# Performance work log

Hardware: AMD Instinct MI355X
Metric: run time of the kernel (lower is better)

The kernel has to match this reference:

```python
import jax, jax.numpy as jnp
import numpy as np

LAMBDA_INIT = 0.8


def setup_inputs() -> dict:
    key = jax.random.key(0)
    ks = jax.random.split(key, 12)
    B, T, E = 2, 2048, 1024
    H = 8            # num_heads // 2 diff-heads
    HS = 64          # head_size
    DO = 128         # 2 * head_output_dimension (per-head output dim)
    q = jax.random.normal(ks[0], (B, T, E), jnp.float32)
    k = jax.random.normal(ks[1], (B, T, E), jnp.float32)
    v = jax.random.normal(ks[2], (B, T, E), jnp.float32)
    s = E ** -0.5  # linear-layer style init scale
    Wq = jax.random.normal(ks[3], (H, E, 2 * HS), jnp.float32) * s
    Wk = jax.random.normal(ks[4], (H, E, 2 * HS), jnp.float32) * s
    Wv = jax.random.normal(ks[5], (H, E, DO), jnp.float32) * s
    # lambda reparam vectors (scaled 0.1 to keep exp(dot) numerically tame)
    lq1 = jax.random.normal(ks[6], (H, HS), jnp.float32) * 0.1
    lk1 = jax.random.normal(ks[7], (H, HS), jnp.float32) * 0.1
    lq2 = jax.random.normal(ks[8], (H, HS), jnp.float32) * 0.1
    lk2 = jax.random.normal(ks[9], (H, HS), jnp.float32) * 0.1
    Wp = jax.random.normal(ks[10], (H * DO, E), jnp.float32) * (H * DO) ** -0.5
    bp = jnp.zeros((E,), jnp.float32)
    # buffer: tril(ones, diagonal=1); positions where it is 0 get -inf
    mask = jnp.tril(jnp.ones((T, T), jnp.bool_), 1)
    return {"q": q, "k": k, "v": v, "Wq": Wq, "Wk": Wk, "Wv": Wv,
            "lq1": lq1, "lk1": lk1, "lq2": lq2, "lk2": lk2,
            "Wp": Wp, "bp": bp, "mask": mask}


def reference(q, k, v, Wq, Wk, Wv, lq1, lk1, lq2, lk2, Wp, bp, mask):
    B, T, E = q.shape
    H = Wq.shape[0]
    HS = Wq.shape[-1] // 2
    scale = HS ** -0.5
    Q = jnp.einsum('bte,hed->bhtd', q, Wq)   # [B,H,T,2HS]
    K = jnp.einsum('bte,hed->bhtd', k, Wk)
    V = jnp.einsum('bte,hed->bhtd', v, Wv)   # [B,H,T,DO]
    Q1, Q2 = jnp.split(Q, 2, axis=-1)
    K1, K2 = jnp.split(K, 2, axis=-1)
    neg_inf = jnp.float32(-jnp.inf)
    s1 = jnp.einsum('bhtd,bhsd->bhts', Q1, K1) * scale
    s2 = jnp.einsum('bhtd,bhsd->bhts', Q2, K2) * scale
    s1 = jnp.where(mask[:T, :T], s1, neg_inf)
    s2 = jnp.where(mask[:T, :T], s2, neg_inf)
    a1 = jax.nn.softmax(s1, axis=-1)
    a2 = jax.nn.softmax(s2, axis=-1)
    lbd = (jnp.exp(jnp.sum(lq1 * lk1, -1)) - jnp.exp(jnp.sum(lq2 * lk2, -1))
           + LAMBDA_INIT)                     # [H]
    attn = a1 - lbd[None, :, None, None] * a2
    ctx = jnp.einsum('bhts,bhsd->bhtd', attn, V) * (1.0 - LAMBDA_INIT)
    out = ctx.transpose(0, 2, 1, 3).reshape(B, T, -1)  # concat heads
    return out @ Wp + bp
```

## Files before the change

kernel.cpp:

```cpp
#include <hip/hip_runtime.h>
#include <hip/hip_bf16.h>


constexpr int Tn = 2048;
constexpr int En = 1024;
constexpr int Hn = 8;
constexpr float LAMBDA_INIT = 0.8f;
constexpr float QSCALE = 0.18033688011112042f;

typedef __attribute__((ext_vector_type(8))) short short8;
typedef __attribute__((ext_vector_type(4))) short s16x4;
typedef __attribute__((ext_vector_type(4))) float f32x4;

__device__ __forceinline__ short f2bf(float x) {
  union { __hip_bfloat16 h; short s; } u;
  u.h = __float2bfloat16(x);
  return u.s;
}
__device__ __forceinline__ void gload16(const short* g, short* l) {
  __builtin_amdgcn_global_load_lds(
      (const __attribute__((address_space(1))) void*)g,
      (__attribute__((address_space(3))) void*)l, 16, 0, 0);
}

__global__ __launch_bounds__(256)
void qkv_mfma(const float* __restrict__ q, const float* __restrict__ k,
              const float* __restrict__ v,
              const float* __restrict__ Wq, const float* __restrict__ Wk,
              const float* __restrict__ Wv,
              short* __restrict__ Qo, short* __restrict__ Ko,
              short* __restrict__ Vto) {
  __shared__ short As[128 * 32];
  __shared__ short Bs[128 * 32];
  const int which = blockIdx.z;
  const float* X = (which == 0) ? q : (which == 1) ? k : v;
  const float* W = (which == 0) ? Wq : (which == 1) ? Wk : Wv;
  const int head = blockIdx.y;
  const int m0 = blockIdx.x * 128;
  const float* Wh = W + (size_t)head * En * 128;
  const float oscale = (which == 0) ? QSCALE : 1.0f;

  const int tid = threadIdx.x;
  const int lane = tid & 63;
  const int w = tid >> 6, wr = w >> 1, wc = w & 1;
  const int fr = lane & 15, fk = (lane >> 4) * 8;
  const int arow = tid >> 1, ah = (tid & 1) * 16;
  const int bn = tid & 127, bkg = (tid >> 7) * 16;

  f32x4 acc[4][4] = {};

  for (int k0 = 0; k0 < En; k0 += 32) {
    float4 xa[4];
#pragma unroll
    for (int qq = 0; qq < 4; ++qq)
      xa[qq] = *(const float4*)&X[(size_t)(m0 + arow) * En + k0 + ah + qq * 4];
    float xb[16];
#pragma unroll
    for (int j = 0; j < 16; ++j)
      xb[j] = Wh[(size_t)(k0 + bkg + j) * 128 + bn];

    __syncthreads();
    short8 pa0, pa1;
#pragma unroll
    for (int e = 0; e < 4; ++e) {
      pa0[e]     = f2bf(((const float*)&xa[0])[e]);
      pa0[e + 4] = f2bf(((const float*)&xa[1])[e]);
      pa1[e]     = f2bf(((const float*)&xa[2])[e]);
      pa1[e + 4] = f2bf(((const float*)&xa[3])[e]);
    }
    *(short8*)&As[arow * 32 + ah] = pa0;
    *(short8*)&As[arow * 32 + ah + 8] = pa1;
    short8 pb0, pb1;
#pragma unroll
    for (int e = 0; e < 8; ++e) {
      pb0[e] = f2bf(xb[e]);
      pb1[e] = f2bf(xb[e + 8]);
    }
    *(short8*)&Bs[bn * 32 + bkg] = pb0;
    *(short8*)&Bs[bn * 32 + bkg + 8] = pb1;
    __syncthreads();

    short8 a[4], b[4];
#pragma unroll
    for (int i = 0; i < 4; ++i)
      a[i] = *(const short8*)&As[(wr * 64 + i * 16 + fr) * 32 + fk];
#pragma unroll
    for (int j = 0; j < 4; ++j)
      b[j] = *(const short8*)&Bs[(wc * 64 + j * 16 + fr) * 32 + fk];
#pragma unroll
    for (int i = 0; i < 4; ++i)
#pragma unroll
      for (int j = 0; j < 4; ++j)
        acc[i][j] = __builtin_amdgcn_mfma_f32_16x16x32_bf16(a[i], b[j],
                                                            acc[i][j], 0, 0, 0);
  }

  const int crow = (lane >> 4) * 4, ccol = lane & 15;
  if (which == 2) {
#pragma unroll
    for (int i = 0; i < 4; ++i) {
      const int m = m0 + wr * 64 + i * 16 + crow;
      const int bb = m >> 11, t = m & (Tn - 1);
#pragma unroll
      for (int j = 0; j < 4; ++j) {
        const int d = wc * 64 + j * 16 + ccol;
        s16x4 pk;
#pragma unroll
        for (int p = 0; p < 4; ++p) pk[p] = f2bf(acc[i][j][p]);
        *(s16x4*)&Vto[((size_t)(bb * Hn + head) * 128 + d) * Tn + t] = pk;
      }
    }
  } else {
    short* Out = (which == 0) ? Qo : Ko;
#pragma unroll
    for (int i = 0; i < 4; ++i) {
      const int m = m0 + wr * 64 + i * 16 + crow;
      const int bb = m >> 11, t = m & (Tn - 1);
      short* dst = Out + ((size_t)(bb * Hn + head) * Tn + t) * 128;
#pragma unroll
      for (int j = 0; j < 4; ++j) {
        const int d = wc * 64 + j * 16 + ccol;
#pragma unroll
        for (int p = 0; p < 4; ++p)
          dst[(size_t)p * 128 + d] = f2bf(acc[i][j][p] * oscale);
      }
    }
  }
}

__global__ __launch_bounds__(256)
void proj_mfma(const short* __restrict__ Xb, const float* __restrict__ W,
               const float* __restrict__ bias, float* __restrict__ Out) {
  __shared__ short As[128 * 32];
  __shared__ short Bs[128 * 32];
  const int m0 = blockIdx.x * 128;
  const int n0 = blockIdx.y * 128;

  const int tid = threadIdx.x;
  const int lane = tid & 63;
  const int w = tid >> 6, wr = w >> 1, wc = w & 1;
  const int fr = lane & 15, fk = (lane >> 4) * 8;
  const int arow = tid >> 1, ah = (tid & 1) * 16;
  const int bn = tid & 127, bkg = (tid >> 7) * 16;

  f32x4 acc[4][4] = {};

  for (int k0 = 0; k0 < En; k0 += 32) {
    short8 xa0 = *(const short8*)&Xb[(size_t)(m0 + arow) * En + k0 + ah];
    short8 xa1 = *(const short8*)&Xb[(size_t)(m0 + arow) * En + k0 + ah + 8];
    float xb[16];
#pragma unroll
    for (int j = 0; j < 16; ++j)
      xb[j] = W[(size_t)(k0 + bkg + j) * En + n0 + bn];

    __syncthreads();
    *(short8*)&As[arow * 32 + ah] = xa0;
    *(short8*)&As[arow * 32 + ah + 8] = xa1;
    short8 pb0, pb1;
#pragma unroll
    for (int e = 0; e < 8; ++e) {
      pb0[e] = f2bf(xb[e]);
      pb1[e] = f2bf(xb[e + 8]);
    }
    *(short8*)&Bs[bn * 32 + bkg] = pb0;
    *(short8*)&Bs[bn * 32 + bkg + 8] = pb1;
    __syncthreads();

    short8 a[4], b[4];
#pragma unroll
    for (int i = 0; i < 4; ++i)
      a[i] = *(const short8*)&As[(wr * 64 + i * 16 + fr) * 32 + fk];
#pragma unroll
    for (int j = 0; j < 4; ++j)
      b[j] = *(const short8*)&Bs[(wc * 64 + j * 16 + fr) * 32 + fk];
#pragma unroll
    for (int i = 0; i < 4; ++i)
#pragma unroll
      for (int j = 0; j < 4; ++j)
        acc[i][j] = __builtin_amdgcn_mfma_f32_16x16x32_bf16(a[i], b[j],
                                                            acc[i][j], 0, 0, 0);
  }

  const int crow = (lane >> 4) * 4, ccol = lane & 15;
#pragma unroll
  for (int i = 0; i < 4; ++i) {
    const int m = m0 + wr * 64 + i * 16 + crow;
#pragma unroll
    for (int j = 0; j < 4; ++j) {
      const int n = n0 + wc * 64 + j * 16 + ccol;
      const float bv = bias[n];
#pragma unroll
      for (int p = 0; p < 4; ++p)
        Out[(size_t)(m + p) * En + n] = acc[i][j][p] + bv;
    }
  }
}

__global__ __launch_bounds__(256, 4)
void diff_attn7(const short* __restrict__ Qg, const short* __restrict__ Kg,
                const short* __restrict__ Vtg,
                const float* __restrict__ lq1, const float* __restrict__ lk1,
                const float* __restrict__ lq2, const float* __restrict__ lk2,
                short* __restrict__ ctxb) {
  __shared__ __align__(16) short pool[18688];

  const int lin = blockIdx.x;
  const int h = lin & 7;
  const int idx = lin >> 3;
  const int b = idx >> 5;
  const int x = idx & 31;
  const int tid = threadIdx.x;
  const int lane = tid & 63;
  const int w = tid >> 6;
  const int st = w >> 1, wh = w & 1;
  const int fr = lane & 15, hi = lane >> 4;
  const int swz = fr & 7;
  const int swv = (fr ^ (fr >> 2)) & 3;
  const size_t basebh = (size_t)(b * Hn + h) * Tn * 128;

  float lbd;
  {
    float a1 = lq1[h * 64 + lane] * lk1[h * 64 + lane];
    float a2 = lq2[h * 64 + lane] * lk2[h * 64 + lane];
#pragma unroll
    for (int off = 1; off <= 32; off <<= 1) {
      a1 += __shfl_xor(a1, off);
      a2 += __shfl_xor(a2, off);
    }
    lbd = __expf(a1) - __expf(a2) + LAMBDA_INIT;
  }

  int ksrc[2], vsrc[2], dsto[2];
#pragma unroll
  for (int j = 0; j < 2; ++j) {
    const int ob = j * 4096 + tid * 16;
    { const int s = ob >> 8, cp = (ob >> 4) & 15, c = cp ^ (s & 7);
      ksrc[j] = s * 128 + c * 8; }
    { const int d = ob >> 6, cp = (ob >> 4) & 3,
          c = cp ^ ((d ^ (d >> 2)) & 3);
      vsrc[j] = d * Tn + c * 8; }
    dsto[j] = (j * 4096 + w * 1024) >> 1;
  }
  const short* kgb = Kg + basebh;
  const short* vgb = Vtg + basebh;

#define STAGE(BUF, S0)                                                   \
  {                                                                      \
    const short* kb_ = kgb + (size_t)(S0) * 128;                         \
    const short* vb_ = vgb + (S0);                                       \
    _Pragma("unroll") for (int j = 0; j < 2; ++j) {                      \
      gload16(kb_ + ksrc[j], pool + (BUF) * 4096 + dsto[j]);             \
      gload16(vb_ + vsrc[j], pool + 8192 + (BUF) * 4096 + dsto[j]);      \
    }                                                                    \
  }

  short8 ones;
#pragma unroll
  for (int e = 0; e < 8; ++e) ones[e] = (short)0x3F80;
  short* Plw = pool + 16384 + w * 576;

  auto phase = [&](int qi) {
    const int q0 = qi * 32;
    const int NT = min(Tn / 32, qi + 2);
    const int tmin = q0 + wh * 16;
    const int tbase = tmin + hi * 4;

    short8 qf[2];
    {
      const short* qp = Qg + basebh + (size_t)(tmin + fr) * 128 + st * 64;
      qf[0] = *(const short8*)(qp + hi * 8);
      qf[1] = *(const short8*)(qp + 32 + hi * 8);
    }
    f32x4 o[8] = {};
    f32x4 ol = {};

    STAGE(0, 0);
    int cur = 0;
    for (int t = 0; t < NT; ++t) {
      const int s0 = t * 32;
      if (t + 1 < NT) {
        STAGE(cur ^ 1, s0 + 32);
        __builtin_amdgcn_sched_barrier(0);
        asm volatile("s_waitcnt vmcnt(4)" ::: "memory");
        __builtin_amdgcn_sched_barrier(0);
      } else {
        __builtin_amdgcn_sched_barrier(0);
        asm volatile("s_waitcnt vmcnt(0)" ::: "memory");
        __builtin_amdgcn_sched_barrier(0);
      }
      __builtin_amdgcn_s_barrier();

      if (s0 <= tmin + 16) {
        const short* Kb = pool + cur * 4096;
        const short* Vb = pool + 8192 + cur * 4096;
        const bool interior = (tmin - s0) >= 30;

        f32x4 s4[2] = {};
        __builtin_amdgcn_s_setprio(1);
#pragma unroll
        for (int sb = 0; sb < 2; ++sb) {
          const int rb = (sb * 16 + fr) * 128;
#pragma unroll
          for (int kp = 0; kp < 2; ++kp) {
            const short8 kb = *(const short8*)
                &Kb[rb + ((st * 8 + ((kp * 4 + hi) ^ swz)) << 3)];
            s4[sb] = __builtin_amdgcn_mfma_f32_16x16x32_bf16(qf[kp], kb,
                                                             s4[sb], 0, 0, 0);
          }
        }
        __builtin_amdgcn_s_setprio(0);
        if (!interior) {
#pragma unroll
          for (int sb = 0; sb < 2; ++sb) {
            const int sg = s0 + sb * 16 + fr;
#pragma unroll
            for (int p = 0; p < 4; ++p)
              if (sg > tbase + p + 1) s4[sb][p] = -1e30f;
          }
        }

#pragma unroll
        for (int sb = 0; sb < 2; ++sb)
#pragma unroll
          for (int p = 0; p < 4; ++p)
            Plw[(hi * 4 + p) * 36 + sb * 16 + fr] =
                f2bf(exp2f(s4[sb][p] - 12.0f));

        const short8 pf = *(const short8*)&Plw[fr * 36 + hi * 8];
        __builtin_amdgcn_s_setprio(1);
        ol = __builtin_amdgcn_mfma_f32_16x16x32_bf16(ones, pf, ol, 0, 0, 0);
#pragma unroll
        for (int dblk = 0; dblk < 8; ++dblk) {
          const short8 va = *(const short8*)
              &Vb[(dblk * 16 + fr) * 32 + ((hi ^ swv) << 3)];
          o[dblk] = __builtin_amdgcn_mfma_f32_16x16x32_bf16(va, pf, o[dblk],
                                                            0, 0, 0);
        }
        __builtin_amdgcn_s_setprio(0);
      }

      __builtin_amdgcn_s_barrier();
      cur ^= 1;
    }

    const float lr = ol[0];
    float* O2L = (float*)pool;
    if (st == 1) {
      const float c2 = (1.0f - LAMBDA_INIT) * lbd / lr;
#pragma unroll
      for (int dblk = 0; dblk < 8; ++dblk)
#pragma unroll
        for (int e = 0; e < 4; ++e)
          O2L[wh * 2176 + (dblk * 16 + hi * 4 + e) * 17 + fr] =
              c2 * o[dblk][e];
    }
    __syncthreads();
    if (st == 0) {
      const float c1 = (1.0f - LAMBDA_INIT) / lr;
      const int t = tmin + fr;
      short* dst = ctxb + ((size_t)b * Tn + t) * En + h * 128;
#pragma unroll
      for (int dblk = 0; dblk < 8; ++dblk) {
        s16x4 pk;
#pragma unroll
        for (int e = 0; e < 4; ++e)
          pk[e] = f2bf(c1 * o[dblk][e] -
                       O2L[wh * 2176 + (dblk * 16 + hi * 4 + e) * 17 + fr]);
        *(s16x4*)&dst[dblk * 16 + hi * 4] = pk;
      }
    }
    __syncthreads();
  };

  phase(63 - x);
  phase(x);
#undef STAGE
}

extern "C" void kernel_launch(void* const* d_in, const int* in_sizes, int n_in,
                              void* d_out, int out_size, void* d_ws, size_t ws_size,
                              hipStream_t stream) {
  const float* q   = (const float*)d_in[0];
  const float* k   = (const float*)d_in[1];
  const float* v   = (const float*)d_in[2];
  const float* Wq  = (const float*)d_in[3];
  const float* Wk  = (const float*)d_in[4];
  const float* Wv  = (const float*)d_in[5];
  const float* lq1 = (const float*)d_in[6];
  const float* lk1 = (const float*)d_in[7];
  const float* lq2 = (const float*)d_in[8];
  const float* lk2 = (const float*)d_in[9];
  const float* Wp  = (const float*)d_in[10];
  const float* bp  = (const float*)d_in[11];

  short* ws = (short*)d_ws;
  const size_t SZ = (size_t)2 * Hn * Tn * 128;
  short* Qb   = ws;
  short* Kb   = ws + SZ;
  short* Vtb  = ws + 2 * SZ;
  short* ctxb = ws + 3 * SZ;

  qkv_mfma<<<dim3(32, 8, 3), dim3(256), 0, stream>>>(q, k, v, Wq, Wk, Wv,
                                                     Qb, Kb, Vtb);
  diff_attn7<<<dim3(512), dim3(256), 0, stream>>>(Qb, Kb, Vtb,
                                                  lq1, lk1, lq2, lk2, ctxb);
  proj_mfma<<<dim3(32, 8), dim3(256), 0, stream>>>(ctxb, Wp, bp,
                                                   (float*)d_out);
}
```

Before: 161.8 us.

## Pipeline K/V loads in pairs of tiles with four-deep LDS ring buffer

The attention kernel's K/V staging goes from a double buffer with one tile per iteration to a four-slot ring. Each iteration now waits once, issues loads for the next two tiles and computes two tiles, which halves the barriers and wait points per phase. This doubles LDS use and lowers the occupancy hint from 4 to 2 blocks per CU. Prefetch past the end is clamped to the last tile, so some redundant loads are issued.

```diff
diff --git a/kernel.cpp b/kernel.cpp
--- a/kernel.cpp
+++ b/kernel.cpp
@@ -196,13 +196,13 @@
   }
 }
 
-__global__ __launch_bounds__(256, 4)
-void diff_attn7(const short* __restrict__ Qg, const short* __restrict__ Kg,
+__global__ __launch_bounds__(256, 2)
+void diff_attn9(const short* __restrict__ Qg, const short* __restrict__ Kg,
                 const short* __restrict__ Vtg,
                 const float* __restrict__ lq1, const float* __restrict__ lk1,
                 const float* __restrict__ lq2, const float* __restrict__ lk2,
                 short* __restrict__ ctxb) {
-  __shared__ __align__(16) short pool[18688];
+  __shared__ __align__(16) short pool[35072];
 
   const int lin = blockIdx.x;
   const int h = lin & 7;
@@ -244,24 +244,27 @@
   const short* kgb = Kg + basebh;
   const short* vgb = Vtg + basebh;
 
-#define STAGE(BUF, S0)                                                   \
+#define STAGE(T)                                                         \
   {                                                                      \
-    const short* kb_ = kgb + (size_t)(S0) * 128;                         \
-    const short* vb_ = vgb + (S0);                                       \
+    const int ts_ = min((T), 63);                                        \
+    const int bf_ = (T) & 3;                                             \
+    const short* kb_ = kgb + (size_t)(ts_ * 32) * 128;                   \
+    const short* vb_ = vgb + ts_ * 32;                                   \
     _Pragma("unroll") for (int j = 0; j < 2; ++j) {                      \
-      gload16(kb_ + ksrc[j], pool + (BUF) * 4096 + dsto[j]);             \
-      gload16(vb_ + vsrc[j], pool + 8192 + (BUF) * 4096 + dsto[j]);      \
+      gload16(kb_ + ksrc[j], pool + bf_ * 4096 + dsto[j]);               \
+      gload16(vb_ + vsrc[j], pool + 16384 + bf_ * 4096 + dsto[j]);       \
     }                                                                    \
   }
 
   short8 ones;
 #pragma unroll
   for (int e = 0; e < 8; ++e) ones[e] = (short)0x3F80;
-  short* Plw = pool + 16384 + w * 576;
+  short* Plw = pool + 32768 + w * 576;
 
   auto phase = [&](int qi) {
     const int q0 = qi * 32;
     const int NT = min(Tn / 32, qi + 2);
+    const int NP = (NT + 1) >> 1;
     const int tmin = q0 + wh * 16;
     const int tbase = tmin + hi * 4;
 
@@ -274,75 +277,73 @@
     f32x4 o[8] = {};
     f32x4 ol = {};
 
-    STAGE(0, 0);
-    int cur = 0;
-    for (int t = 0; t < NT; ++t) {
+    auto tile_compute = [&](int t) {
       const int s0 = t * 32;
-      if (t + 1 < NT) {
-        STAGE(cur ^ 1, s0 + 32);
-        __builtin_amdgcn_sched_barrier(0);
-        asm volatile("s_waitcnt vmcnt(4)" ::: "memory");
-        __builtin_amdgcn_sched_barrier(0);
-      } else {
-        __builtin_amdgcn_sched_barrier(0);
-        asm volatile("s_waitcnt vmcnt(0)" ::: "memory");
-        __builtin_amdgcn_sched_barrier(0);
-      }
+      if (s0 > tmin + 16) return;
+      const short* Kb = pool + (t & 3) * 4096;
+      const short* Vb = pool + 16384 + (t & 3) * 4096;
+      const bool interior = (tmin - s0) >= 30;
+
+      f32x4 s4[2] = {};
+      __builtin_amdgcn_s_setprio(1);
+#pragma unroll
+      for (int sb = 0; sb < 2; ++sb) {
+        const int rb = (sb * 16 + fr) * 128;
+#pragma unroll
+        for (int kp = 0; kp < 2; ++kp) {
+          const short8 kb = *(const short8*)
+              &Kb[rb + ((st * 8 + ((kp * 4 + hi) ^ swz)) << 3)];
+          s4[sb] = __builtin_amdgcn_mfma_f32_16x16x32_bf16(qf[kp], kb,
+                                                           s4[sb], 0, 0, 0);
+        }
+      }
+      __builtin_amdgcn_s_setprio(0);
+      if (!interior) {
+#pragma unroll
+        for (int sb = 0; sb < 2; ++sb) {
+          const int sg = s0 + sb * 16 + fr;
+#pragma unroll
+          for (int p = 0; p < 4; ++p)
+            if (sg > tbase + p + 1) s4[sb][p] = -1e30f;
+        }
+      }
+
+#pragma unroll
+      for (int sb = 0; sb < 2; ++sb)
+#pragma unroll
+        for (int p = 0; p < 4; ++p)
+          Plw[(hi * 4 + p) * 36 + sb * 16 + fr] =
+              f2bf(exp2f(s4[sb][p] - 12.0f));
+
+      const short8 pf = *(const short8*)&Plw[fr * 36 + hi * 8];
+      __builtin_amdgcn_s_setprio(1);
+      ol = __builtin_amdgcn_mfma_f32_16x16x32_bf16(ones, pf, ol, 0, 0, 0);
+#pragma unroll
+      for (int dblk = 0; dblk < 8; ++dblk) {
+        const short8 va = *(const short8*)
+            &Vb[(dblk * 16 + fr) * 32 + ((hi ^ swv) << 3)];
+        o[dblk] = __builtin_amdgcn_mfma_f32_16x16x32_bf16(va, pf, o[dblk],
+                                                          0, 0, 0);
+      }
+      __builtin_amdgcn_s_setprio(0);
+    };
+
+    STAGE(0);
+    STAGE(1);
+    for (int p = 0; p < NP; ++p) {
+      __builtin_amdgcn_sched_barrier(0);
+      asm volatile("s_waitcnt vmcnt(0)" ::: "memory");
+      __builtin_amdgcn_sched_barrier(0);
       __builtin_amdgcn_s_barrier();
 
-      if (s0 <= tmin + 16) {
-        const short* Kb = pool + cur * 4096;
-        const short* Vb = pool + 8192 + cur * 4096;
-        const bool interior = (tmin - s0) >= 30;
-
-        f32x4 s4[2] = {};
-        __builtin_amdgcn_s_setprio(1);
-#pragma unroll
-        for (int sb = 0; sb < 2; ++sb) {
-          const int rb = (sb * 16 + fr) * 128;
-#pragma unroll
-          for (int kp = 0; kp < 2; ++kp) {
-            const short8 kb = *(const short8*)
-                &Kb[rb + ((st * 8 + ((kp * 4 + hi) ^ swz)) << 3)];
-            s4[sb] = __builtin_amdgcn_mfma_f32_16x16x32_bf16(qf[kp], kb,
-                                                             s4[sb], 0, 0, 0);
-          }
-        }
-        __builtin_amdgcn_s_setprio(0);
-        if (!interior) {
-#pragma unroll
-          for (int sb = 0; sb < 2; ++sb) {
-            const int sg = s0 + sb * 16 + fr;
-#pragma unroll
-            for (int p = 0; p < 4; ++p)
-              if (sg > tbase + p + 1) s4[sb][p] = -1e30f;
-          }
-        }
-
-#pragma unroll
-        for (int sb = 0; sb < 2; ++sb)
-#pragma unroll
-          for (int p = 0; p < 4; ++p)
-            Plw[(hi * 4 + p) * 36 + sb * 16 + fr] =
-                f2bf(exp2f(s4[sb][p] - 12.0f));
-
-        const short8 pf = *(const short8*)&Plw[fr * 36 + hi * 8];
-        __builtin_amdgcn_s_setprio(1);
-        ol = __builtin_amdgcn_mfma_f32_16x16x32_bf16(ones, pf, ol, 0, 0, 0);
-#pragma unroll
-        for (int dblk = 0; dblk < 8; ++dblk) {
-          const short8 va = *(const short8*)
-              &Vb[(dblk * 16 + fr) * 32 + ((hi ^ swv) << 3)];
-          o[dblk] = __builtin_amdgcn_mfma_f32_16x16x32_bf16(va, pf, o[dblk],
-                                                            0, 0, 0);
-        }
-        __builtin_amdgcn_s_setprio(0);
-      }
-
-      __builtin_amdgcn_s_barrier();
-      cur ^= 1;
-    }
-
+      STAGE(2 * p + 2);
+      STAGE(2 * p + 3);
+
+      tile_compute(2 * p);
+      if (2 * p + 1 < NT) tile_compute(2 * p + 1);
+    }
+
+    __builtin_amdgcn_s_barrier();
     const float lr = ol[0];
     float* O2L = (float*)pool;
     if (st == 1) {
@@ -402,7 +403,7 @@
 
   qkv_mfma<<<dim3(32, 8, 3), dim3(256), 0, stream>>>(q, k, v, Wq, Wk, Wv,
                                                      Qb, Kb, Vtb);
-  diff_attn7<<<dim3(512), dim3(256), 0, stream>>>(Qb, Kb, Vtb,
+  diff_attn9<<<dim3(512), dim3(256), 0, stream>>>(Qb, Kb, Vtb,
                                                   lq1, lk1, lq2, lk2, ctxb);
   proj_mfma<<<dim3(32, 8), dim3(256), 0, stream>>>(ctxb, Wp, bp,
                                                    (float*)d_out);
```

Result: no change. 163.6 us (+1.1%).

## Double-buffer LDS in QKV and projection GEMMs; halve projection M-tile

Applied to the files above, without the earlier changes.

Both the QKV projection and the output projection GEMMs now keep two LDS buffers and register-prefetch the next K-slice. The next tile is converted and written while MFMAs run on the current one, so only one barrier per iteration remains. The projection kernel also shrinks its M tile from 128 to 64 rows and doubles its grid to 512 blocks, which gives more blocks across the CUs. The cost is more LDS per block, more registers held by prefetch, and more reloading of the W matrix in the projection.

```diff
diff --git a/kernel.cpp b/kernel.cpp
--- a/kernel.cpp
+++ b/kernel.cpp
@@ -30,8 +30,8 @@
               const float* __restrict__ Wv,
               short* __restrict__ Qo, short* __restrict__ Ko,
               short* __restrict__ Vto) {
-  __shared__ short As[128 * 32];
-  __shared__ short Bs[128 * 32];
+  __shared__ short As[2][128 * 32];
+  __shared__ short Bs[2][128 * 32];
   const int which = blockIdx.z;
   const float* X = (which == 0) ? q : (which == 1) ? k : v;
   const float* W = (which == 0) ? Wq : (which == 1) ? Wk : Wv;
@@ -47,19 +47,18 @@
   const int arow = tid >> 1, ah = (tid & 1) * 16;
   const int bn = tid & 127, bkg = (tid >> 7) * 16;
 
-  f32x4 acc[4][4] = {};
-
-  for (int k0 = 0; k0 < En; k0 += 32) {
-    float4 xa[4];
+  float4 xa[4];
+  float xb[16];
+
+  auto gload = [&](int k0) {
 #pragma unroll
     for (int qq = 0; qq < 4; ++qq)
       xa[qq] = *(const float4*)&X[(size_t)(m0 + arow) * En + k0 + ah + qq * 4];
-    float xb[16];
 #pragma unroll
     for (int j = 0; j < 16; ++j)
       xb[j] = Wh[(size_t)(k0 + bkg + j) * 128 + bn];
-
-    __syncthreads();
+  };
+  auto cvtwrite = [&](int buf) {
     short8 pa0, pa1;
 #pragma unroll
     for (int e = 0; e < 4; ++e) {
@@ -68,31 +67,44 @@
       pa1[e]     = f2bf(((const float*)&xa[2])[e]);
       pa1[e + 4] = f2bf(((const float*)&xa[3])[e]);
     }
-    *(short8*)&As[arow * 32 + ah] = pa0;
-    *(short8*)&As[arow * 32 + ah + 8] = pa1;
+    *(short8*)&As[buf][arow * 32 + ah] = pa0;
+    *(short8*)&As[buf][arow * 32 + ah + 8] = pa1;
     short8 pb0, pb1;
 #pragma unroll
     for (int e = 0; e < 8; ++e) {
       pb0[e] = f2bf(xb[e]);
       pb1[e] = f2bf(xb[e + 8]);
     }
-    *(short8*)&Bs[bn * 32 + bkg] = pb0;
-    *(short8*)&Bs[bn * 32 + bkg + 8] = pb1;
-    __syncthreads();
-
+    *(short8*)&Bs[buf][bn * 32 + bkg] = pb0;
+    *(short8*)&Bs[buf][bn * 32 + bkg + 8] = pb1;
+  };
+
+  f32x4 acc[4][4] = {};
+  gload(0);
+  cvtwrite(0);
+  gload(32);
+  __syncthreads();
+
+  for (int k0 = 0; k0 < En; k0 += 32) {
+    const int cur = (k0 >> 5) & 1;
+    if (k0 + 32 < En) {
+      cvtwrite(cur ^ 1);
+      if (k0 + 64 < En) gload(k0 + 64);
+    }
     short8 a[4], b[4];
 #pragma unroll
     for (int i = 0; i < 4; ++i)
-      a[i] = *(const short8*)&As[(wr * 64 + i * 16 + fr) * 32 + fk];
+      a[i] = *(const short8*)&As[cur][(wr * 64 + i * 16 + fr) * 32 + fk];
 #pragma unroll
     for (int j = 0; j < 4; ++j)
-      b[j] = *(const short8*)&Bs[(wc * 64 + j * 16 + fr) * 32 + fk];
+      b[j] = *(const short8*)&Bs[cur][(wc * 64 + j * 16 + fr) * 32 + fk];
 #pragma unroll
     for (int i = 0; i < 4; ++i)
 #pragma unroll
       for (int j = 0; j < 4; ++j)
         acc[i][j] = __builtin_amdgcn_mfma_f32_16x16x32_bf16(a[i], b[j],
                                                             acc[i][j], 0, 0, 0);
+    __syncthreads();
   }
 
   const int crow = (lane >> 4) * 4, ccol = lane & 15;
@@ -131,60 +143,71 @@
 __global__ __launch_bounds__(256)
 void proj_mfma(const short* __restrict__ Xb, const float* __restrict__ W,
                const float* __restrict__ bias, float* __restrict__ Out) {
-  __shared__ short As[128 * 32];
-  __shared__ short Bs[128 * 32];
-  const int m0 = blockIdx.x * 128;
+  __shared__ short As[2][64 * 32];
+  __shared__ short Bs[2][128 * 32];
+  const int m0 = blockIdx.x * 64;
   const int n0 = blockIdx.y * 128;
 
   const int tid = threadIdx.x;
   const int lane = tid & 63;
   const int w = tid >> 6, wr = w >> 1, wc = w & 1;
   const int fr = lane & 15, fk = (lane >> 4) * 8;
-  const int arow = tid >> 1, ah = (tid & 1) * 16;
+  const int arow = tid >> 2, ah = (tid & 3) * 8;
   const int bn = tid & 127, bkg = (tid >> 7) * 16;
 
-  f32x4 acc[4][4] = {};
-
-  for (int k0 = 0; k0 < En; k0 += 32) {
-    short8 xa0 = *(const short8*)&Xb[(size_t)(m0 + arow) * En + k0 + ah];
-    short8 xa1 = *(const short8*)&Xb[(size_t)(m0 + arow) * En + k0 + ah + 8];
-    float xb[16];
+  short8 xa8;
+  float xb[16];
+
+  auto gload = [&](int k0) {
+    xa8 = *(const short8*)&Xb[(size_t)(m0 + arow) * En + k0 + ah];
 #pragma unroll
     for (int j = 0; j < 16; ++j)
       xb[j] = W[(size_t)(k0 + bkg + j) * En + n0 + bn];
-
-    __syncthreads();
-    *(short8*)&As[arow * 32 + ah] = xa0;
-    *(short8*)&As[arow * 32 + ah + 8] = xa1;
+  };
+  auto cvtwrite = [&](int buf) {
+    *(short8*)&As[buf][arow * 32 + ah] = xa8;
     short8 pb0, pb1;
 #pragma unroll
     for (int e = 0; e < 8; ++e) {
       pb0[e] = f2bf(xb[e]);
       pb1[e] = f2bf(xb[e + 8]);
     }
-    *(short8*)&Bs[bn * 32 + bkg] = pb0;
-    *(short8*)&Bs[bn * 32 + bkg + 8] = pb1;
-    __syncthreads();
-
-    short8 a[4], b[4];
-#pragma unroll
-    for (int i = 0; i < 4; ++i)
-      a[i] = *(const short8*)&As[(wr * 64 + i * 16 + fr) * 32 + fk];
+    *(short8*)&Bs[buf][bn * 32 + bkg] = pb0;
+    *(short8*)&Bs[buf][bn * 32 + bkg + 8] = pb1;
+  };
+
+  f32x4 acc[2][4] = {};
+  gload(0);
+  cvtwrite(0);
+  gload(32);
+  __syncthreads();
+
+  for (int k0 = 0; k0 < En; k0 += 32) {
+    const int cur = (k0 >> 5) & 1;
+    if (k0 + 32 < En) {
+      cvtwrite(cur ^ 1);
+      if (k0 + 64 < En) gload(k0 + 64);
+    }
+    short8 a[2], b[4];
+#pragma unroll
+    for (int i = 0; i < 2; ++i)
+      a[i] = *(const short8*)&As[cur][(wr * 32 + i * 16 + fr) * 32 + fk];
 #pragma unroll
     for (int j = 0; j < 4; ++j)
-      b[j] = *(const short8*)&Bs[(wc * 64 + j * 16 + fr) * 32 + fk];
-#pragma unroll
-    for (int i = 0; i < 4; ++i)
+      b[j] = *(const short8*)&Bs[cur][(wc * 64 + j * 16 + fr) * 32 + fk];
+#pragma unroll
+    for (int i = 0; i < 2; ++i)
 #pragma unroll
       for (int j = 0; j < 4; ++j)
         acc[i][j] = __builtin_amdgcn_mfma_f32_16x16x32_bf16(a[i], b[j],
                                                             acc[i][j], 0, 0, 0);
+    __syncthreads();
   }
 
   const int crow = (lane >> 4) * 4, ccol = lane & 15;
 #pragma unroll
-  for (int i = 0; i < 4; ++i) {
-    const int m = m0 + wr * 64 + i * 16 + crow;
+  for (int i = 0; i < 2; ++i) {
+    const int m = m0 + wr * 32 + i * 16 + crow;
 #pragma unroll
     for (int j = 0; j < 4; ++j) {
       const int n = n0 + wc * 64 + j * 16 + ccol;
@@ -404,6 +427,6 @@
                                                      Qb, Kb, Vtb);
   diff_attn7<<<dim3(512), dim3(256), 0, stream>>>(Qb, Kb, Vtb,
                                                   lq1, lk1, lq2, lk2, ctxb);
-  proj_mfma<<<dim3(32, 8), dim3(256), 0, stream>>>(ctxb, Wp, bp,
+  proj_mfma<<<dim3(64, 8), dim3(256), 0, stream>>>(ctxb, Wp, bp,
                                                    (float*)d_out);
 }
```

Measured after the change: 161.3 us. About the same (-0.3%).
